# Kernel optimization log

Measured on AMD Instinct MI355X. Metric: run time of the kernel, lower is better.

## Reference

```python
import jax, jax.numpy as jnp
from jax import lax
import numpy as np

DYADIC_ORDER = 1  # matches init_kwargs


def _solve_pde_last(vf):
    """Goursat PDE solve (2nd-order explicit scheme, as in sigkernel/sigkax).
    vf: (m, n) vector field (refined double increments of the static kernel).
    Returns K[m, n], i.e. the bottom-right corner of the (m+1, n+1) solution
    grid with boundary K[0,:] = K[:,0] = 1 and recurrence
        K[i+1,j+1] = (K[i+1,j] + K[i,j+1]) * (1 + vf/2 + vf^2/12)
                     - K[i,j] * (1 - vf^2/12).
    Implemented as a row scan with an inner column scan (the column recurrence
    is first-order linear in K[i+1, j]).
    """
    m, n = vf.shape
    c1 = 1.0 + 0.5 * vf + (vf * vf) / 12.0  # (m, n)
    c2 = 1.0 - (vf * vf) / 12.0             # (m, n)

    def row_step(prev_row, row_coeffs):
        c1_r, c2_r = row_coeffs  # each (n,)

        def col_step(k_left, inp):
            c1j, c2j, kp_j, kp_j1 = inp
            k_new = c1j * (k_left + kp_j1) - c2j * kp_j
            return k_new, k_new

        _, tail = lax.scan(col_step, jnp.float32(1.0),
                           (c1_r, c2_r, prev_row[:-1], prev_row[1:]))
        new_row = jnp.concatenate([jnp.ones((1,), vf.dtype), tail])
        return new_row, None

    row0 = jnp.ones((n + 1,), vf.dtype)
    last_row, _ = lax.scan(row_step, row0, (c1, c2))
    return last_row[-1]


def _sig_kernel(xs, ys, dyadic_order):
    d = 2 ** dyadic_order
    # static (linear) kernel for every pair: (Bx, By, Lx, Ly)
    k = jnp.einsum('ald,bmd->ablm', xs, ys)
    # finite_diff: double increments, scaled by 1/(2^d)^2, dyadically refined
    inc = (k[..., 1:, 1:] - k[..., 1:, :-1]
           - k[..., :-1, 1:] + k[..., :-1, :-1]) / float(d * d)
    vf = jnp.repeat(jnp.repeat(inc, d, axis=-2), d, axis=-1)
    bx, by, m, n = vf.shape
    sol = jax.vmap(_solve_pde_last)(vf.reshape(bx * by, m, n))
    return sol.reshape(bx, by)


def setup_inputs() -> dict:
    key = jax.random.key(0)
    kx, ky = jax.random.split(key)
    # scale 0.1 keeps path increments small so the multiplicative PDE
    # solution stays numerically tame (signature kernels grow exponentially)
    xs = 0.1 * jax.random.normal(kx, (32, 64, 16), dtype=jnp.float32)
    ys = 0.1 * jax.random.normal(ky, (32, 64, 16), dtype=jnp.float32)
    return {"xs": xs, "ys": ys}


def reference(xs, ys):
    return _sig_kernel(xs, ys, DYADIC_ORDER)
```

## Files before the change

### kernel.cpp

```cpp
#include <hip/hip_runtime.h>


#define NL 64
#define ND 16
#define NQ 63
#define SDXH_STR 12
#define CO_STR 64

typedef _Float16 half2_t __attribute__((ext_vector_type(2)));

__device__ __forceinline__ half2_t cvt_pk_f16(float a, float b) {
    return __builtin_bit_cast(half2_t, __builtin_amdgcn_cvt_pkrtz(a, b));
}

__device__ __forceinline__ float dpp_shr1_old1(float x, float one) {
    int r = __builtin_amdgcn_update_dpp(__float_as_int(one), __float_as_int(x),
                                        0x138, 0xf, 0xf, false);
    return __int_as_float(r);
}

__global__ void __launch_bounds__(64)
sig_pde_kernel(const float* __restrict__ xs,
               const float* __restrict__ ys,
               float* __restrict__ out)
{
    __shared__ int    sdxh[NQ * SDXH_STR];
    __shared__ float2 coef[65 * CO_STR];

    const int a = blockIdx.y;
    const int b = blockIdx.x;
    const int p = threadIdx.x;

    const float* xa = xs + a * (NL * ND);
    const float* yb = ys + b * (NL * ND);

    half2_t hy0, hy1, hy2, hy3, hy4, hy5, hy6, hy7;
    hy0 = hy1 = hy2 = hy3 = hy4 = hy5 = hy6 = hy7 = half2_t(0);

    if (p < NQ) {
        const float4* x0 = reinterpret_cast<const float4*>(xa + p * ND);
        const float4* x1 = reinterpret_cast<const float4*>(xa + (p + 1) * ND);
        const float4* y0 = reinterpret_cast<const float4*>(yb + p * ND);
        const float4* y1 = reinterpret_cast<const float4*>(yb + (p + 1) * ND);
        int dxw[8];
#pragma unroll
        for (int e = 0; e < 4; ++e) {
            float4 u = x1[e], v = x0[e];
            dxw[2 * e]     = __builtin_bit_cast(int, cvt_pk_f16(u.x - v.x, u.y - v.y));
            dxw[2 * e + 1] = __builtin_bit_cast(int, cvt_pk_f16(u.z - v.z, u.w - v.w));
        }
        int4* dst = reinterpret_cast<int4*>(&sdxh[p * SDXH_STR]);
        dst[0] = make_int4(dxw[0], dxw[1], dxw[2], dxw[3]);
        dst[1] = make_int4(dxw[4], dxw[5], dxw[6], dxw[7]);
        float4 s, t;
        s = y0[0]; t = y1[0];
        hy0 = cvt_pk_f16(t.x - s.x, t.y - s.y);
        hy1 = cvt_pk_f16(t.z - s.z, t.w - s.w);
        s = y0[1]; t = y1[1];
        hy2 = cvt_pk_f16(t.x - s.x, t.y - s.y);
        hy3 = cvt_pk_f16(t.z - s.z, t.w - s.w);
        s = y0[2]; t = y1[2];
        hy4 = cvt_pk_f16(t.x - s.x, t.y - s.y);
        hy5 = cvt_pk_f16(t.z - s.z, t.w - s.w);
        s = y0[3]; t = y1[3];
        hy6 = cvt_pk_f16(t.x - s.x, t.y - s.y);
        hy7 = cvt_pk_f16(t.z - s.z, t.w - s.w);
    }
    coef[0 * CO_STR + p]  = make_float2(0.5f, 0.f);
    coef[64 * CO_STR + p] = make_float2(0.5f, 0.f);
    __syncthreads();

#pragma unroll 7
    for (int q = 0; q < NQ; ++q) {
        const int4* rw = reinterpret_cast<const int4*>(&sdxh[q * SDXH_STR]);
        int4 w0 = rw[0], w1 = rw[1];
        float dot = __builtin_amdgcn_fdot2(__builtin_bit_cast(half2_t, w0.x), hy0, 0.f,  false);
        dot = __builtin_amdgcn_fdot2(__builtin_bit_cast(half2_t, w0.y), hy1, dot, false);
        dot = __builtin_amdgcn_fdot2(__builtin_bit_cast(half2_t, w0.z), hy2, dot, false);
        dot = __builtin_amdgcn_fdot2(__builtin_bit_cast(half2_t, w0.w), hy3, dot, false);
        dot = __builtin_amdgcn_fdot2(__builtin_bit_cast(half2_t, w1.x), hy4, dot, false);
        dot = __builtin_amdgcn_fdot2(__builtin_bit_cast(half2_t, w1.y), hy5, dot, false);
        dot = __builtin_amdgcn_fdot2(__builtin_bit_cast(half2_t, w1.z), hy6, dot, false);
        dot = __builtin_amdgcn_fdot2(__builtin_bit_cast(half2_t, w1.w), hy7, dot, false);
        const float v  = 0.25f * dot;
        const float v2 = v * v * (1.0f / 12.0f);
        const float c1 = __builtin_fmaf(0.5f, v, 1.f) + v2;
        const float c2 = 1.f - v2;
        coef[(q + 1) * CO_STR + p] = make_float2(c1, c2);
    }

    const float one = 1.0f;
    float kA1 = 1.f;
    float kB1 = 1.f;
    float bM  = 1.f;
    float rx  = 1.f;

    const float2* cp = &coef[p];
    auto ldrow = [&](int q1) -> float2 {
        unsigned rc = (unsigned)q1 > 64u ? 64u : (unsigned)q1;
        return cp[rc * CO_STR];
    };

    float2 cb0 = ldrow(1 - p);
    float2 cb1 = ldrow(2 - p);
    float2 cb2 = ldrow(3 - p);
    float2 cb3 = ldrow(4 - p);
    float2 cb4 = ldrow(5 - p);

#pragma unroll 5
    for (int T = 0; T < 125; ++T) {
        float2 cbn = ldrow(T + 6 - p);
        const float nbB = dpp_shr1_old1(kB1, one);
        const float nbM = dpp_shr1_old1(bM,  one);
        const float c1 = cb0.x, c2 = cb0.y;

        const float a11 = __builtin_fmaf(c1, nbM + kA1, -(c2 * rx));
        const float a12 = __builtin_fmaf(c1, a11 + kB1, -(c2 * kA1));
        const float a21 = __builtin_fmaf(c1, nbB + a11, -(c2 * nbM));
        const float a22 = __builtin_fmaf(c1, a21 + a12, -(c2 * a11));

        rx = nbB; bM = a12; kA1 = a21; kB1 = a22;
        cb0 = cb1; cb1 = cb2; cb2 = cb3; cb3 = cb4; cb4 = cbn;
    }

    if (p == 62) {
        out[a * 32 + b] = kB1;
    }
}

extern "C" void kernel_launch(void* const* d_in, const int* in_sizes, int n_in,
                              void* d_out, int out_size, void* d_ws, size_t ws_size,
                              hipStream_t stream)
{
    const float* xs = (const float*)d_in[0];
    const float* ys = (const float*)d_in[1];
    float* out = (float*)d_out;

    dim3 grid(32, 32, 1);
    dim3 block(64, 1, 1);
    hipLaunchKernelGGL(sig_pde_kernel, grid, block, 0, stream, xs, ys, out);
}
```

Before: 14.96 us.

## Compute double-increment coefficients with MFMA 16x16x32 instead of per-lane fdot2 loop

Replaces the 63-iteration per-lane fdot2 loop that builds the PDE coefficient table with sixteen MFMA f16 16x16x32 tiles, which compute the full 64x64 increment Gram matrix. Both x and y increments are staged in LDS, zero-padded to K=32 and to 64 rows, and that staging area is aliased onto the coefficient buffer. The scaling constants are folded into the c1/c2 formulas. This adds an extra barrier and scattered LDS stores per tile. Row 64 of the coefficient table now comes from zero-padded data (c1=1, c2=1) instead of (0.5, 0).

```diff
diff --git a/kernel.cpp b/kernel.cpp
--- a/kernel.cpp
+++ b/kernel.cpp
@@ -4,13 +4,19 @@
 #define NL 64
 #define ND 16
 #define NQ 63
-#define SDXH_STR 12
 #define CO_STR 64
+#define XW 20
 
+typedef _Float16 f16x8 __attribute__((ext_vector_type(8)));
+typedef float    f32x4 __attribute__((ext_vector_type(4)));
 typedef _Float16 half2_t __attribute__((ext_vector_type(2)));
 
 __device__ __forceinline__ half2_t cvt_pk_f16(float a, float b) {
     return __builtin_bit_cast(half2_t, __builtin_amdgcn_cvt_pkrtz(a, b));
+}
+
+__device__ __forceinline__ int pack_f16(float a, float b) {
+    return __builtin_bit_cast(int, cvt_pk_f16(a, b));
 }
 
 __device__ __forceinline__ float dpp_shr1_old1(float x, float one) {
@@ -24,8 +30,10 @@
                const float* __restrict__ ys,
                float* __restrict__ out)
 {
-    __shared__ int    sdxh[NQ * SDXH_STR];
-    __shared__ float2 coef[65 * CO_STR];
+    __shared__ __align__(16) char lds[65 * CO_STR * 8];
+    float2* coef = reinterpret_cast<float2*>(lds);
+    int*    dxw  = reinterpret_cast<int*>(lds);
+    int*    dyw  = reinterpret_cast<int*>(lds + 64 * XW * 4);
 
     const int a = blockIdx.y;
     const int b = blockIdx.x;
@@ -34,60 +42,77 @@
     const float* xa = xs + a * (NL * ND);
     const float* yb = ys + b * (NL * ND);
 
-    half2_t hy0, hy1, hy2, hy3, hy4, hy5, hy6, hy7;
-    hy0 = hy1 = hy2 = hy3 = hy4 = hy5 = hy6 = hy7 = half2_t(0);
-
-    if (p < NQ) {
-        const float4* x0 = reinterpret_cast<const float4*>(xa + p * ND);
-        const float4* x1 = reinterpret_cast<const float4*>(xa + (p + 1) * ND);
-        const float4* y0 = reinterpret_cast<const float4*>(yb + p * ND);
-        const float4* y1 = reinterpret_cast<const float4*>(yb + (p + 1) * ND);
-        int dxw[8];
+    {
+        const int  rlo  = (p < 62) ? p : 62;
+        const bool real = (p < NQ);
+        const float4* x0 = reinterpret_cast<const float4*>(xa + rlo * ND);
+        const float4* x1 = reinterpret_cast<const float4*>(xa + (rlo + 1) * ND);
+        const float4* y0 = reinterpret_cast<const float4*>(yb + rlo * ND);
+        const float4* y1 = reinterpret_cast<const float4*>(yb + (rlo + 1) * ND);
+        int dwx[8], dwy[8];
 #pragma unroll
         for (int e = 0; e < 4; ++e) {
             float4 u = x1[e], v = x0[e];
-            dxw[2 * e]     = __builtin_bit_cast(int, cvt_pk_f16(u.x - v.x, u.y - v.y));
-            dxw[2 * e + 1] = __builtin_bit_cast(int, cvt_pk_f16(u.z - v.z, u.w - v.w));
+            dwx[2 * e]     = real ? pack_f16(u.x - v.x, u.y - v.y) : 0;
+            dwx[2 * e + 1] = real ? pack_f16(u.z - v.z, u.w - v.w) : 0;
+            float4 s = y0[e], t = y1[e];
+            dwy[2 * e]     = real ? pack_f16(t.x - s.x, t.y - s.y) : 0;
+            dwy[2 * e + 1] = real ? pack_f16(t.z - s.z, t.w - s.w) : 0;
         }
-        int4* dst = reinterpret_cast<int4*>(&sdxh[p * SDXH_STR]);
-        dst[0] = make_int4(dxw[0], dxw[1], dxw[2], dxw[3]);
-        dst[1] = make_int4(dxw[4], dxw[5], dxw[6], dxw[7]);
-        float4 s, t;
-        s = y0[0]; t = y1[0];
-        hy0 = cvt_pk_f16(t.x - s.x, t.y - s.y);
-        hy1 = cvt_pk_f16(t.z - s.z, t.w - s.w);
-        s = y0[1]; t = y1[1];
-        hy2 = cvt_pk_f16(t.x - s.x, t.y - s.y);
-        hy3 = cvt_pk_f16(t.z - s.z, t.w - s.w);
-        s = y0[2]; t = y1[2];
-        hy4 = cvt_pk_f16(t.x - s.x, t.y - s.y);
-        hy5 = cvt_pk_f16(t.z - s.z, t.w - s.w);
-        s = y0[3]; t = y1[3];
-        hy6 = cvt_pk_f16(t.x - s.x, t.y - s.y);
-        hy7 = cvt_pk_f16(t.z - s.z, t.w - s.w);
+        int4* dx4 = reinterpret_cast<int4*>(&dxw[p * XW]);
+        dx4[0] = make_int4(dwx[0], dwx[1], dwx[2], dwx[3]);
+        dx4[1] = make_int4(dwx[4], dwx[5], dwx[6], dwx[7]);
+        dx4[2] = make_int4(0, 0, 0, 0);
+        dx4[3] = make_int4(0, 0, 0, 0);
+        int4* dy4 = reinterpret_cast<int4*>(&dyw[p * XW]);
+        dy4[0] = make_int4(dwy[0], dwy[1], dwy[2], dwy[3]);
+        dy4[1] = make_int4(dwy[4], dwy[5], dwy[6], dwy[7]);
+        dy4[2] = make_int4(0, 0, 0, 0);
+        dy4[3] = make_int4(0, 0, 0, 0);
     }
-    coef[0 * CO_STR + p]  = make_float2(0.5f, 0.f);
-    coef[64 * CO_STR + p] = make_float2(0.5f, 0.f);
     __syncthreads();
 
-#pragma unroll 7
-    for (int q = 0; q < NQ; ++q) {
-        const int4* rw = reinterpret_cast<const int4*>(&sdxh[q * SDXH_STR]);
-        int4 w0 = rw[0], w1 = rw[1];
-        float dot = __builtin_amdgcn_fdot2(__builtin_bit_cast(half2_t, w0.x), hy0, 0.f,  false);
-        dot = __builtin_amdgcn_fdot2(__builtin_bit_cast(half2_t, w0.y), hy1, dot, false);
-        dot = __builtin_amdgcn_fdot2(__builtin_bit_cast(half2_t, w0.z), hy2, dot, false);
-        dot = __builtin_amdgcn_fdot2(__builtin_bit_cast(half2_t, w0.w), hy3, dot, false);
-        dot = __builtin_amdgcn_fdot2(__builtin_bit_cast(half2_t, w1.x), hy4, dot, false);
-        dot = __builtin_amdgcn_fdot2(__builtin_bit_cast(half2_t, w1.y), hy5, dot, false);
-        dot = __builtin_amdgcn_fdot2(__builtin_bit_cast(half2_t, w1.z), hy6, dot, false);
-        dot = __builtin_amdgcn_fdot2(__builtin_bit_cast(half2_t, w1.w), hy7, dot, false);
-        const float v  = 0.25f * dot;
-        const float v2 = v * v * (1.0f / 12.0f);
-        const float c1 = __builtin_fmaf(0.5f, v, 1.f) + v2;
-        const float c2 = 1.f - v2;
-        coef[(q + 1) * CO_STR + p] = make_float2(c1, c2);
+    const int g   = p >> 4;
+    const int r16 = p & 15;
+    f16x8 Af0, Af1, Af2, Af3, Bf0, Bf1, Bf2, Bf3;
+    {
+        const int base = r16 * XW + 4 * g;
+        Af0 = __builtin_bit_cast(f16x8, *reinterpret_cast<const int4*>(&dxw[base]));
+        Af1 = __builtin_bit_cast(f16x8, *reinterpret_cast<const int4*>(&dxw[base + 16 * XW]));
+        Af2 = __builtin_bit_cast(f16x8, *reinterpret_cast<const int4*>(&dxw[base + 32 * XW]));
+        Af3 = __builtin_bit_cast(f16x8, *reinterpret_cast<const int4*>(&dxw[base + 48 * XW]));
+        Bf0 = __builtin_bit_cast(f16x8, *reinterpret_cast<const int4*>(&dyw[base]));
+        Bf1 = __builtin_bit_cast(f16x8, *reinterpret_cast<const int4*>(&dyw[base + 16 * XW]));
+        Bf2 = __builtin_bit_cast(f16x8, *reinterpret_cast<const int4*>(&dyw[base + 32 * XW]));
+        Bf3 = __builtin_bit_cast(f16x8, *reinterpret_cast<const int4*>(&dyw[base + 48 * XW]));
     }
+    __syncthreads();
+
+    coef[p] = make_float2(0.5f, 0.f);
+
+    {
+        f16x8 Afs[4] = {Af0, Af1, Af2, Af3};
+        f16x8 Bfs[4] = {Bf0, Bf1, Bf2, Bf3};
+        float2* crow = coef + (4 * g + 1) * CO_STR + r16;
+#pragma unroll
+        for (int ti = 0; ti < 4; ++ti) {
+#pragma unroll
+            for (int tj = 0; tj < 4; ++tj) {
+                f32x4 acc = {0.f, 0.f, 0.f, 0.f};
+                acc = __builtin_amdgcn_mfma_f32_16x16x32_f16(Afs[ti], Bfs[tj], acc, 0, 0, 0);
+#pragma unroll
+                for (int r = 0; r < 4; ++r) {
+                    const float dot = acc[r];
+                    const float d2  = dot * dot;
+                    const float c1  = __builtin_fmaf(d2, (1.f / 192.f),
+                                      __builtin_fmaf(dot, 0.125f, 1.f));
+                    const float c2  = __builtin_fmaf(d2, (-1.f / 192.f), 1.f);
+                    crow[(16 * ti + r) * CO_STR + 16 * tj] = make_float2(c1, c2);
+                }
+            }
+        }
+    }
+    __syncthreads();
 
     const float one = 1.0f;
     float kA1 = 1.f;
```

Result: faster. 13.63 us (-8.9%).
